# Optimization experiments

Measured on AMD Instinct MI355X. Metric: run time of the kernel, lower is better.

The kernel has to match this reference:

```python
import jax, jax.numpy as jnp
import numpy as np

Q_DIM = 256
CTX_DIM = 256
FF_DIM = 1024
B, LQ, LKV = 8, 2048, 4096


def setup_inputs() -> dict:
    key = jax.random.key(0)
    ks = jax.random.split(key, 16)
    s = lambda d: 1.0 / np.sqrt(d)
    return {
        "query": jax.random.normal(ks[0], (B, LQ, Q_DIM), jnp.float32),
        "key": jax.random.normal(ks[1], (B, LKV, CTX_DIM), jnp.float32),
        "value": jax.random.normal(ks[2], (B, LKV, CTX_DIM), jnp.float32),
        # attention projections (stored [in, out])
        "Wk": jax.random.normal(ks[3], (CTX_DIM, Q_DIM), jnp.float32) * s(CTX_DIM),
        "bk": jnp.zeros((Q_DIM,), jnp.float32),
        "Wv": jax.random.normal(ks[4], (CTX_DIM, Q_DIM), jnp.float32) * s(CTX_DIM),
        "bv": jnp.zeros((Q_DIM,), jnp.float32),
        "Wo": jax.random.normal(ks[5], (Q_DIM, Q_DIM), jnp.float32) * s(Q_DIM),
        "bo": jnp.zeros((Q_DIM,), jnp.float32),
        # layernorms
        "g1": jnp.ones((Q_DIM,), jnp.float32),
        "b1": jnp.zeros((Q_DIM,), jnp.float32),
        "g2": jnp.ones((Q_DIM,), jnp.float32),
        "b2": jnp.zeros((Q_DIM,), jnp.float32),
        # feedforward
        "W1": jax.random.normal(ks[6], (Q_DIM, FF_DIM), jnp.float32) * s(Q_DIM),
        "bf1": jnp.zeros((FF_DIM,), jnp.float32),
        "W2": jax.random.normal(ks[7], (FF_DIM, Q_DIM), jnp.float32) * s(FF_DIM),
        "bf2": jnp.zeros((Q_DIM,), jnp.float32),
    }


def _layernorm(x, g, b, eps=1e-5):
    mu = jnp.mean(x, axis=-1, keepdims=True)
    var = jnp.var(x, axis=-1, keepdims=True)
    return (x - mu) * jax.lax.rsqrt(var + eps) * g + b


def reference(query, key, value, Wk, bk, Wv, bv, Wo, bo, g1, b1, g2, b2, W1, bf1, W2, bf2):
    # CrossAttention (single-head, naive)
    key_proj = key @ Wk + bk        # [B, Lkv, D]
    value_proj = value @ Wv + bv    # [B, Lkv, D]
    scale = 1.0 / jnp.sqrt(jnp.asarray(Q_DIM, query.dtype))
    scores = jnp.einsum("bqd,bkd->bqk", query, key_proj) * scale  # [B, Lq, Lkv]
    weights = jax.nn.softmax(scores, axis=-1)
    context = jnp.einsum("bqk,bkd->bqd", weights, value_proj)     # [B, Lq, D]
    attn_out = context @ Wo + bo
    # residual + LN
    x = _layernorm(query + attn_out, g1, b1)
    # FeedForward (condition_dim=0, dropout=0)
    ff = jax.nn.relu(x @ W1 + bf1) @ W2 + bf2
    return _layernorm(x + ff, g2, b2)
```

## Files before the change

kernel.cpp:

```cpp
#include <hip/hip_runtime.h>
#include <stdint.h>

typedef __attribute__((ext_vector_type(4))) float f32x4;
typedef __attribute__((ext_vector_type(16))) float f32x16;
typedef __attribute__((ext_vector_type(8))) short short8;
typedef __attribute__((ext_vector_type(4))) short short4v;
typedef __attribute__((ext_vector_type(4))) unsigned uint4v;

__device__ __forceinline__ short f2bf(float f) {
  union { float f; uint32_t u; } v; v.f = f;
  uint32_t r = v.u + 0x7FFFu + ((v.u >> 16) & 1u);
  return (short)(r >> 16);
}

__device__ __forceinline__ float bf2f(short s) {
  union { unsigned u; float f; } v; v.u = ((unsigned)(unsigned short)s) << 16; return v.f;
}

__device__ __forceinline__ unsigned cvt_pk_bf16(float lo, float hi) {
  unsigned r;
  asm("v_cvt_pk_bf16_f32 %0, %1, %2" : "=v"(r) : "v"(lo), "v"(hi));
  return r;
}

__device__ __forceinline__ void pl32swap(unsigned& x, unsigned& y) {
  asm volatile("v_permlane32_swap_b32 %0, %1" : "+v"(x), "+v"(y));
}

__device__ __forceinline__ f32x4 mfma16(short8 a, short8 b, f32x4 c) {
  return __builtin_amdgcn_mfma_f32_16x16x32_bf16(a, b, c, 0, 0, 0);
}
__device__ __forceinline__ f32x16 mfma32(short8 a, short8 b, f32x16 c) {
  return __builtin_amdgcn_mfma_f32_32x32x16_bf16(a, b, c, 0, 0, 0);
}

#define NB 8
#define LQ 2048
#define LKV 4096
#define DQ 256
#define FF 1024
#define NCHUNK 2
#define ROWS (NB * LQ)

#define AS1(p) ((const __attribute__((address_space(1))) void*)(p))
#define AS3(p) ((__attribute__((address_space(3))) void*)(p))

__global__ void transpose_all(
    const float* __restrict__ Wk, const float* __restrict__ Wv,
    const float* __restrict__ Wo, const float* __restrict__ W1,
    const float* __restrict__ W2,
    short* __restrict__ WkT, short* __restrict__ WvT, short* __restrict__ WoT,
    short* __restrict__ W1T, short* __restrict__ W2T) {
  __shared__ float t[32][33];
  int bid = blockIdx.x;
  const float* in; short* out; int R, C, b0;
  if (bid < 64)       { in = Wk; out = WkT; R = 256;  C = 256;  b0 = bid; }
  else if (bid < 128) { in = Wv; out = WvT; R = 256;  C = 256;  b0 = bid - 64; }
  else if (bid < 192) { in = Wo; out = WoT; R = 256;  C = 256;  b0 = bid - 128; }
  else if (bid < 448) { in = W1; out = W1T; R = 256;  C = 1024; b0 = bid - 192; }
  else                { in = W2; out = W2T; R = 1024; C = 256;  b0 = bid - 448; }
  int nbx = C / 32;
  int c0 = (b0 % nbx) * 32, r0 = (b0 / nbx) * 32;
  int tx = threadIdx.x, ty = threadIdx.y;
#pragma unroll
  for (int dy = 0; dy < 32; dy += 8)
    t[ty + dy][tx] = in[(long)(r0 + ty + dy) * C + c0 + tx];
  __syncthreads();
#pragma unroll
  for (int dy = 0; dy < 32; dy += 8)
    out[(long)(c0 + ty + dy) * R + r0 + tx] = f2bf(t[tx][ty + dy]);
}

template <int AMODE, int BMODE, int EPI>
__global__ void __launch_bounds__(256, 2) gemm128(
    const void* __restrict__ A, long sAb, int lda,
    const void* __restrict__ B, long sBb, int ldb,
    const float* __restrict__ bias,
    void* C, long sCb, int ldc, int K) {
  __shared__ char lds[32768];
  const int tid = threadIdx.x;
  const int bn = blockIdx.x, bm = blockIdx.y, bz = blockIdx.z;
  const int w = tid >> 6, l = tid & 63;
  const int wm = w & 1, wn = w >> 1;
  const int lr = l & 15, lq = l >> 4;

  auto stageReg = [&](const float* src, int ld, long row0, int k0, char* ldsb) {
#pragma unroll
    for (int it = 0; it < 4; ++it) {
      int idx = it * 2048 + tid * 8;
      int r = idx >> 6, c = idx & 63;
      const float* p = src + (row0 + r) * (long)ld + k0 + c;
      f32x4 f0 = *(const f32x4*)p, f1 = *(const f32x4*)(p + 4);
      uint4v u;
      u[0] = cvt_pk_bf16(f0[0], f0[1]); u[1] = cvt_pk_bf16(f0[2], f0[3]);
      u[2] = cvt_pk_bf16(f1[0], f1[1]); u[3] = cvt_pk_bf16(f1[2], f1[3]);
      *(short8*)(ldsb + ((r * 128 + c * 2) ^ ((r & 7) << 4))) = *(short8*)&u;
    }
  };
  auto stageGld = [&](const short* src, int ld, long row0, int k0, char* ldsb) {
#pragma unroll
    for (int it = 0; it < 4; ++it) {
      const int span = it * 4096 + w * 1024;
      int idx = (span >> 4) + l;
      int r = idx >> 3, c = idx & 7;
      __builtin_amdgcn_global_load_lds(
          AS1(src + (row0 + r) * (long)ld + k0 + ((c ^ (r & 7)) * 8)),
          AS3(ldsb + span), 16, 0, 0);
    }
  };

  f32x4 acc[4][4] = {};
  for (int k0 = 0; k0 < K; k0 += 64) {
    if (AMODE == 0)      stageGld((const short*)A + sAb * bz, lda, (long)bm * 128, k0, lds);
    else                 stageReg((const float*)A + sAb * bz, lda, (long)bm * 128, k0, lds);
    if (BMODE == 0)      stageGld((const short*)B + sBb * bz, ldb, (long)bn * 128, k0, lds + 16384);
    else                 stageReg((const float*)B + sBb * bz, ldb, (long)bn * 128, k0, lds + 16384);
    __syncthreads();
    short8 af[4][2], bfr[4][2];
#pragma unroll
    for (int i = 0; i < 4; ++i) {
#pragma unroll
      for (int kk = 0; kk < 2; ++kk) {
        int ra = wm * 64 + i * 16 + lr;
        af[i][kk] = *(const short8*)(lds + ((ra * 128 + (kk * 32 + lq * 8) * 2) ^ ((ra & 7) << 4)));
        int rb = wn * 64 + i * 16 + lr;
        bfr[i][kk] = *(const short8*)(lds + 16384 + ((rb * 128 + (kk * 32 + lq * 8) * 2) ^ ((rb & 7) << 4)));
      }
    }
#pragma unroll
    for (int i = 0; i < 4; ++i)
#pragma unroll
      for (int j = 0; j < 4; ++j) {
        acc[i][j] = mfma16(af[i][0], bfr[j][0], acc[i][j]);
        acc[i][j] = mfma16(af[i][1], bfr[j][1], acc[i][j]);
      }
    __syncthreads();
  }
#pragma unroll
  for (int i = 0; i < 4; ++i) {
#pragma unroll
    for (int j = 0; j < 4; ++j) {
#pragma unroll
      for (int r = 0; r < 4; ++r) {
        long row = (long)bm * 128 + wm * 64 + i * 16 + lq * 4 + r;
        long col = (long)bn * 128 + wn * 64 + j * 16 + lr;
        float v = acc[i][j][r];
        if (EPI == 0) {
          v += bias[col];
          ((short*)C + sCb * bz)[row * ldc + col] = f2bf(v);
        } else if (EPI == 1) {
          v += bias[row];
          ((short*)C + sCb * bz)[row * ldc + col] = f2bf(v);
        } else {
          v += bias[col];
          v = fmaxf(v, 0.f);
          ((short*)C + sCb * bz)[row * ldc + col] = f2bf(v);
        }
      }
    }
  }
}

template <int AMODE, bool RESF32, bool WF32, bool WB16>
__global__ void __launch_bounds__(256, 2) gemmln(
    const void* __restrict__ A, const short* __restrict__ Bw,
    const float* __restrict__ bias, const void* __restrict__ resid,
    const float* __restrict__ Mcomb, const float* __restrict__ Lcomb,
    const float* __restrict__ g, const float* __restrict__ be,
    float* __restrict__ outF, short* __restrict__ outB, int K) {
  __shared__ char lds[40960];
  const int tid = threadIdx.x;
  const int bm = blockIdx.x;
  const int w = tid >> 6, l = tid & 63;
  const int lr = l & 15, lq = l >> 4;
  char* ldsA = lds;
  char* ldsB = lds + 8192;

  f32x4 acc[16] = {};
  for (int k0 = 0; k0 < K; k0 += 64) {
    if (AMODE == 0) {
      const short* src = (const short*)A;
#pragma unroll
      for (int it = 0; it < 2; ++it) {
        const int span = it * 4096 + w * 1024;
        int idx = (span >> 4) + l;
        int r = idx >> 3, c = idx & 7;
        __builtin_amdgcn_global_load_lds(
            AS1(src + ((long)bm * 64 + r) * K + k0 + ((c ^ (r & 7)) * 8)),
            AS3(ldsA + span), 16, 0, 0);
      }
    } else {
      const short* O0 = (const short*)A;
#pragma unroll
      for (int it = 0; it < 2; ++it) {
        int idx = it * 2048 + tid * 8;
        int r = idx >> 6, c = idx & 63;
        long row = (long)bm * 64 + r;
        float m0 = Mcomb[row], m1 = Mcomb[ROWS + row];
        float l0 = Lcomb[row], l1 = Lcomb[ROWS + row];
        float M = fmaxf(m0, m1);
        float e0 = exp2f(m0 - M) * l0, e1 = exp2f(m1 - M) * l1;
        float inv = 1.f / (e0 + e1);
        float w0 = e0 * inv, w1 = e1 * inv;
        const short* p0 = O0 + row * 256 + k0 + c;
        short8 v0 = *(const short8*)p0;
        short8 v1 = *(const short8*)(p0 + (long)ROWS * 256);
        uint4v u;
#pragma unroll
        for (int j = 0; j < 4; ++j) {
          float x0 = w0 * bf2f(v0[2 * j])     + w1 * bf2f(v1[2 * j]);
          float x1 = w0 * bf2f(v0[2 * j + 1]) + w1 * bf2f(v1[2 * j + 1]);
          u[j] = cvt_pk_bf16(x0, x1);
        }
        *(short8*)(ldsA + ((r * 128 + c * 2) ^ ((r & 7) << 4))) = *(short8*)&u;
      }
    }
#pragma unroll
    for (int it = 0; it < 8; ++it) {
      const int span = it * 4096 + w * 1024;
      int idx = (span >> 4) + l;
      int r = idx >> 3, c = idx & 7;
      __builtin_amdgcn_global_load_lds(
          AS1(Bw + (long)r * K + k0 + ((c ^ (r & 7)) * 8)),
          AS3(ldsB + span), 16, 0, 0);
    }
    __syncthreads();
    short8 af0, af1;
    {
      int ra = w * 16 + lr;
      af0 = *(const short8*)(ldsA + ((ra * 128 + (lq * 8) * 2) ^ ((ra & 7) << 4)));
      af1 = *(const short8*)(ldsA + ((ra * 128 + (32 + lq * 8) * 2) ^ ((ra & 7) << 4)));
    }
#pragma unroll
    for (int j = 0; j < 16; ++j) {
      int rb = j * 16 + lr;
      short8 b0 = *(const short8*)(ldsB + ((rb * 128 + (lq * 8) * 2) ^ ((rb & 7) << 4)));
      short8 b1 = *(const short8*)(ldsB + ((rb * 128 + (32 + lq * 8) * 2) ^ ((rb & 7) << 4)));
      acc[j] = mfma16(af0, b0, acc[j]);
      acc[j] = mfma16(af1, b1, acc[j]);
    }
    __syncthreads();
  }

  const long rowbase = (long)bm * 64 + w * 16;
  float bia[16], gg[16], bb[16];
#pragma unroll
  for (int j = 0; j < 16; ++j) {
    int col = j * 16 + lr;
    bia[j] = bias[col]; gg[j] = g[col]; bb[j] = be[col];
  }
#pragma unroll
  for (int r = 0; r < 4; ++r) {
    long row = rowbase + lq * 4 + r;
    float v[16];
    float s = 0.f, s2 = 0.f;
#pragma unroll
    for (int j = 0; j < 16; ++j) {
      long idx = row * 256 + j * 16 + lr;
      float rx = RESF32 ? ((const float*)resid)[idx] : bf2f(((const short*)resid)[idx]);
      float x = acc[j][r] + bia[j] + rx;
      v[j] = x; s += x; s2 += x * x;
    }
#pragma unroll
    for (int mk = 1; mk < 16; mk <<= 1) { s += __shfl_xor(s, mk); s2 += __shfl_xor(s2, mk); }
    float mu = s * (1.f / 256.f);
    float var = s2 * (1.f / 256.f) - mu * mu;
    float rstd = rsqrtf(var + 1e-5f);
#pragma unroll
    for (int j = 0; j < 16; ++j) {
      int col = j * 16 + lr;
      float y = (v[j] - mu) * rstd * gg[j] + bb[j];
      if (WF32) outF[row * 256 + col] = y;
      if (WB16) outB[row * 256 + col] = f2bf(y);
    }
  }
}

__global__ void __launch_bounds__(256, 1) flash_attn(
    const float* __restrict__ Q, const short* __restrict__ Kb,
    const short* __restrict__ Vt, short* __restrict__ Opart,
    float* __restrict__ Mb, float* __restrict__ Lb) {
  __shared__ char lds[131072];
  const int tid = threadIdx.x;
  const int n = blockIdx.x;
  const int b = n & 7;
  const int slot = n >> 3;
  const int qt = slot & 15;
  const int ch = slot >> 4;
  const int wid = tid >> 6, l = tid & 63;
  const int ql = l & 31, h = l >> 5;
  const int qrow0 = qt * 128 + wid * 32;
  const float* Qp = Q + ((long)b * LQ + qrow0 + ql) * DQ;
  const short* Kp = Kb + (long)b * LKV * DQ;
  const short* Vp = Vt + (long)b * DQ * LKV;
  const float SCQ = 0.0625f * 1.4426950408889634f;

  auto stage = [&](int bufb, int kv0) {
    char* kqb = lds + bufb * 65536;
    char* vtb = kqb + 32768;
#pragma unroll
    for (int i = 0; i < 8; ++i) {
      const int j = wid * 8192 + i * 1024;
      {
        int r = (j >> 9) + (l >> 5);
        int cc = l & 31;
        const short* gk = Kp + (long)(kv0 + r) * DQ + ((cc ^ (r & 15)) * 8);
        __builtin_amdgcn_global_load_lds(AS1(gk), AS3(kqb + j), 16, 0, 0);
      }
      {
        int d = (j >> 7) + (l >> 3);
        int cc = l & 7;
        const short* gv = Vp + (long)d * LKV + kv0 + ((cc ^ (d & 7)) * 8);
        __builtin_amdgcn_global_load_lds(AS1(gv), AS3(vtb + j), 16, 0, 0);
      }
    }
  };

  short8 qf[16];
#pragma unroll
  for (int w = 0; w < 16; ++w) {
    const float* p = Qp + w * 16 + h * 8;
    f32x4 f0 = *(const f32x4*)p, f1 = *(const f32x4*)(p + 4);
    short8 v;
#pragma unroll
    for (int j = 0; j < 4; ++j) { v[j] = f2bf(f0[j] * SCQ); v[4 + j] = f2bf(f1[j] * SCQ); }
    qf[w] = v;
  }

  f32x16 o[8] = {};
  float m_r = -1e30f, l_r = 0.f;

  const int kv_lo = ch * (LKV / NCHUNK);
  const int NT = (LKV / NCHUNK) / 64;

  stage(0, kv_lo);

  for (int t = 0; t < NT; ++t) {
    if (t + 1 < NT) {
      stage((t + 1) & 1, kv_lo + (t + 1) * 64);
      asm volatile("s_waitcnt vmcnt(16)" ::: "memory");
    } else {
      asm volatile("s_waitcnt vmcnt(0)" ::: "memory");
    }
    __builtin_amdgcn_s_barrier();
    __builtin_amdgcn_sched_barrier(0);
    char* kq = lds + (t & 1) * 65536;
    char* vt = kq + 32768;

    f32x16 sa = {}, sb = {};
    {
      const int krA = ql, krB = 32 + ql;
      const int baseA = krA * 512, swzA = (krA & 15) << 4;
      const int baseB = krB * 512, swzB = (krB & 15) << 4;
#pragma unroll
      for (int w = 0; w < 16; ++w) {
        short8 kfA = *(const short8*)(kq + ((baseA + w * 32 + h * 16) ^ swzA));
        sa = mfma32(kfA, qf[w], sa);
        short8 kfB = *(const short8*)(kq + ((baseB + w * 32 + h * 16) ^ swzB));
        sb = mfma32(kfB, qf[w], sb);
      }
    }

    {
      float m8[8];
#pragma unroll
      for (int i = 0; i < 8; ++i)
        m8[i] = fmaxf(fmaxf(sa[i], sa[i + 8]), fmaxf(sb[i], sb[i + 8]));
      float m0 = fmaxf(fmaxf(m8[0], m8[1]), fmaxf(m8[2], m8[3]));
      float m1 = fmaxf(fmaxf(m8[4], m8[5]), fmaxf(m8[6], m8[7]));
      float pmax = fmaxf(m0, m1);
      pmax = fmaxf(pmax, __shfl_xor(pmax, 32));
      if (__any(pmax > m_r + 8.f)) {
        float mn = fmaxf(m_r, pmax);
        float alpha = exp2f(m_r - mn);
        m_r = mn;
        l_r *= alpha;
#pragma unroll
        for (int rr = 0; rr < 16; ++rr) {
          int src = ((rr & 3) + 8 * (rr >> 2) + 4 * h) + 32 * h;
          float ar = __shfl(alpha, src);
#pragma unroll
          for (int nn = 0; nn < 8; ++nn) o[nn][rr] *= ar;
        }
      }
    }

    short8 paA[2], paB[2];
    float rs0 = 0.f, rs1 = 0.f, rs2 = 0.f, rs3 = 0.f;
    {
      float pA[16];
#pragma unroll
      for (int i = 0; i < 16; ++i) pA[i] = exp2f(sa[i] - m_r);
#pragma unroll
      for (int i = 0; i < 4; ++i) { rs0 += pA[4 * i]; rs1 += pA[4 * i + 1]; rs2 += pA[4 * i + 2]; rs3 += pA[4 * i + 3]; }
#pragma unroll
      for (int v = 0; v < 2; ++v) {
        unsigned w01 = cvt_pk_bf16(pA[8 * v + 0], pA[8 * v + 1]);
        unsigned w23 = cvt_pk_bf16(pA[8 * v + 2], pA[8 * v + 3]);
        unsigned w45 = cvt_pk_bf16(pA[8 * v + 4], pA[8 * v + 5]);
        unsigned w67 = cvt_pk_bf16(pA[8 * v + 6], pA[8 * v + 7]);
        pl32swap(w01, w45);
        pl32swap(w23, w67);
        uint4v u = {w01, w23, w45, w67};
        paA[v] = *(short8*)&u;
      }
    }
    {
      float pB[16];
#pragma unroll
      for (int i = 0; i < 16; ++i) pB[i] = exp2f(sb[i] - m_r);
#pragma unroll
      for (int i = 0; i < 4; ++i) { rs0 += pB[4 * i]; rs1 += pB[4 * i + 1]; rs2 += pB[4 * i + 2]; rs3 += pB[4 * i + 3]; }
#pragma unroll
      for (int v = 0; v < 2; ++v) {
        unsigned w01 = cvt_pk_bf16(pB[8 * v + 0], pB[8 * v + 1]);
        unsigned w23 = cvt_pk_bf16(pB[8 * v + 2], pB[8 * v + 3]);
        unsigned w45 = cvt_pk_bf16(pB[8 * v + 4], pB[8 * v + 5]);
        unsigned w67 = cvt_pk_bf16(pB[8 * v + 6], pB[8 * v + 7]);
        pl32swap(w01, w45);
        pl32swap(w23, w67);
        uint4v u = {w01, w23, w45, w67};
        paB[v] = *(short8*)&u;
      }
    }
    {
      float rs = (rs0 + rs1) + (rs2 + rs3);
      rs += __shfl_xor(rs, 32);
      l_r += rs;
    }

#pragma unroll
    for (int nn = 0; nn < 8; ++nn) {
      const int d = 32 * nn + ql;
      const int dbase = d * 128, dswz = (d & 7) << 4;
      short8 bv0 = *(const short8*)(vt + ((dbase + 0 * 32 + 16 * h) ^ dswz));
      o[nn] = mfma32(paA[0], bv0, o[nn]);
      short8 bv1 = *(const short8*)(vt + ((dbase + 1 * 32 + 16 * h) ^ dswz));
      o[nn] = mfma32(paA[1], bv1, o[nn]);
      short8 bv2 = *(const short8*)(vt + ((dbase + 2 * 32 + 16 * h) ^ dswz));
      o[nn] = mfma32(paB[0], bv2, o[nn]);
      short8 bv3 = *(const short8*)(vt + ((dbase + 3 * 32 + 16 * h) ^ dswz));
      o[nn] = mfma32(paB[1], bv3, o[nn]);
    }

    asm volatile("s_waitcnt lgkmcnt(0)" ::: "memory");
    __builtin_amdgcn_s_barrier();
    __builtin_amdgcn_sched_barrier(0);
  }

  const long rowb = (long)b * LQ + qrow0;
  float inv_l = 1.f / l_r;
#pragma unroll
  for (int rr = 0; rr < 16; ++rr) {
    int rloc = (rr & 3) + 8 * (rr >> 2) + 4 * h;
    float li = __shfl(inv_l, rloc + 32 * h);
    long grow = rowb + rloc;
    short* dst = Opart + ((long)ch * ROWS + grow) * 256 + ql;
#pragma unroll
    for (int nn = 0; nn < 8; ++nn) dst[32 * nn] = f2bf(o[nn][rr] * li);
  }
  if (h == 0) {
    Mb[(long)ch * ROWS + rowb + ql] = m_r;
    Lb[(long)ch * ROWS + rowb + ql] = l_r;
  }
}

extern "C" void kernel_launch(void* const* d_in, const int* in_sizes, int n_in,
                              void* d_out, int out_size, void* d_ws, size_t ws_size,
                              hipStream_t stream) {
  const float* query = (const float*)d_in[0];
  const float* key   = (const float*)d_in[1];
  const float* value = (const float*)d_in[2];
  const float* Wk  = (const float*)d_in[3];
  const float* bk  = (const float*)d_in[4];
  const float* Wv  = (const float*)d_in[5];
  const float* bv  = (const float*)d_in[6];
  const float* Wo  = (const float*)d_in[7];
  const float* bo  = (const float*)d_in[8];
  const float* g1  = (const float*)d_in[9];
  const float* b1  = (const float*)d_in[10];
  const float* g2  = (const float*)d_in[11];
  const float* b2  = (const float*)d_in[12];
  const float* W1  = (const float*)d_in[13];
  const float* bf1 = (const float*)d_in[14];
  const float* W2  = (const float*)d_in[15];
  const float* bf2 = (const float*)d_in[16];

  char* ws = (char*)d_ws;
  size_t off = 0;
  auto take = [&](size_t bytes) { char* p = ws + off; off += bytes; return p; };
  short* WkT = (short*)take((size_t)256 * 256 * 2);
  short* WvT = (short*)take((size_t)256 * 256 * 2);
  short* WoT = (short*)take((size_t)256 * 256 * 2);
  short* W1T = (short*)take((size_t)1024 * 256 * 2);
  short* W2T = (short*)take((size_t)256 * 1024 * 2);
  short* Kb  = (short*)take((size_t)NB * LKV * DQ * 2);
  short* Vt  = (short*)take((size_t)NB * DQ * LKV * 2);
  short* Opart = (short*)take((size_t)NCHUNK * ROWS * 256 * 2);
  float* Mbuf  = (float*)take((size_t)NCHUNK * ROWS * 4);
  float* Lbuf  = (float*)take((size_t)NCHUNK * ROWS * 4);
  short* Xb    = (short*)take((size_t)ROWS * 256 * 2);
  short* Hb  = (short*)Kb;
  (void)ws_size; (void)in_sizes; (void)n_in; (void)out_size;

  dim3 blk(256);
  transpose_all<<<dim3(704), dim3(32, 8), 0, stream>>>(
      Wk, Wv, Wo, W1, W2, WkT, WvT, WoT, W1T, W2T);

  gemm128<1, 0, 0><<<dim3(2, 256, 1), blk, 0, stream>>>(
      key, 0, 256, WkT, 0, 256, bk, Kb, 0, 256, 256);
  gemm128<0, 1, 1><<<dim3(32, 2, 8), blk, 0, stream>>>(
      WvT, 0, 256, value, (long)LKV * 256, 256, bv, Vt, (long)256 * LKV, LKV, 256);
  flash_attn<<<dim3(256), blk, 0, stream>>>(query, Kb, Vt, Opart, Mbuf, Lbuf);
  gemmln<2, true, false, true><<<dim3(ROWS / 64), blk, 0, stream>>>(
      Opart, WoT, bo, query, Mbuf, Lbuf, g1, b1, nullptr, Xb, 256);
  gemm128<0, 0, 3><<<dim3(8, 128, 1), blk, 0, stream>>>(
      Xb, 0, 256, W1T, 0, 256, bf1, Hb, 0, 1024, 256);
  gemmln<0, false, true, false><<<dim3(ROWS / 64), blk, 0, stream>>>(
      Hb, W2T, bf2, Xb, nullptr, nullptr, g2, b2, (float*)d_out, nullptr, 1024);
}
```

Measured before the change: 222.2 us.

## Double-buffer LDS staging in gemmln for the direct-load A mode

For AMODE 0, the gemmln kernel now splits LDS into two 40 KB buffers and prefetches the next K-slice of A and the weights with global_load_lds while the current slice runs through MFMA. It uses a partial vmcnt wait and raw s_barrier calls in place of two __syncthreads per iteration. The goal is to hide global-load latency behind compute. In exchange, LDS per block doubles to 80 KB, which may cut the two-blocks-per-CU occupancy set by the launch bounds.

```diff
diff --git a/kernel.cpp b/kernel.cpp
--- a/kernel.cpp
+++ b/kernel.cpp
@@ -168,53 +168,25 @@
     const float* __restrict__ Mcomb, const float* __restrict__ Lcomb,
     const float* __restrict__ g, const float* __restrict__ be,
     float* __restrict__ outF, short* __restrict__ outB, int K) {
-  __shared__ char lds[40960];
+  __shared__ char lds[(AMODE == 0) ? 81920 : 40960];
   const int tid = threadIdx.x;
   const int bm = blockIdx.x;
   const int w = tid >> 6, l = tid & 63;
   const int lr = l & 15, lq = l >> 4;
-  char* ldsA = lds;
-  char* ldsB = lds + 8192;
-
-  f32x4 acc[16] = {};
-  for (int k0 = 0; k0 < K; k0 += 64) {
-    if (AMODE == 0) {
-      const short* src = (const short*)A;
-#pragma unroll
-      for (int it = 0; it < 2; ++it) {
-        const int span = it * 4096 + w * 1024;
-        int idx = (span >> 4) + l;
-        int r = idx >> 3, c = idx & 7;
-        __builtin_amdgcn_global_load_lds(
-            AS1(src + ((long)bm * 64 + r) * K + k0 + ((c ^ (r & 7)) * 8)),
-            AS3(ldsA + span), 16, 0, 0);
-      }
-    } else {
-      const short* O0 = (const short*)A;
-#pragma unroll
-      for (int it = 0; it < 2; ++it) {
-        int idx = it * 2048 + tid * 8;
-        int r = idx >> 6, c = idx & 63;
-        long row = (long)bm * 64 + r;
-        float m0 = Mcomb[row], m1 = Mcomb[ROWS + row];
-        float l0 = Lcomb[row], l1 = Lcomb[ROWS + row];
-        float M = fmaxf(m0, m1);
-        float e0 = exp2f(m0 - M) * l0, e1 = exp2f(m1 - M) * l1;
-        float inv = 1.f / (e0 + e1);
-        float w0 = e0 * inv, w1 = e1 * inv;
-        const short* p0 = O0 + row * 256 + k0 + c;
-        short8 v0 = *(const short8*)p0;
-        short8 v1 = *(const short8*)(p0 + (long)ROWS * 256);
-        uint4v u;
-#pragma unroll
-        for (int j = 0; j < 4; ++j) {
-          float x0 = w0 * bf2f(v0[2 * j])     + w1 * bf2f(v1[2 * j]);
-          float x1 = w0 * bf2f(v0[2 * j + 1]) + w1 * bf2f(v1[2 * j + 1]);
-          u[j] = cvt_pk_bf16(x0, x1);
-        }
-        *(short8*)(ldsA + ((r * 128 + c * 2) ^ ((r & 7) << 4))) = *(short8*)&u;
-      }
-    }
+
+  auto stageA0 = [&](int k0, char* ldsA) {
+    const short* src = (const short*)A;
+#pragma unroll
+    for (int it = 0; it < 2; ++it) {
+      const int span = it * 4096 + w * 1024;
+      int idx = (span >> 4) + l;
+      int r = idx >> 3, c = idx & 7;
+      __builtin_amdgcn_global_load_lds(
+          AS1(src + ((long)bm * 64 + r) * K + k0 + ((c ^ (r & 7)) * 8)),
+          AS3(ldsA + span), 16, 0, 0);
+    }
+  };
+  auto stageB = [&](int k0, char* ldsB) {
 #pragma unroll
     for (int it = 0; it < 8; ++it) {
       const int span = it * 4096 + w * 1024;
@@ -224,13 +196,39 @@
           AS1(Bw + (long)r * K + k0 + ((c ^ (r & 7)) * 8)),
           AS3(ldsB + span), 16, 0, 0);
     }
-    __syncthreads();
+  };
+  auto stageA2 = [&](int k0, char* ldsA) {
+    const short* O0 = (const short*)A;
+#pragma unroll
+    for (int it = 0; it < 2; ++it) {
+      int idx = it * 2048 + tid * 8;
+      int r = idx >> 6, c = idx & 63;
+      long row = (long)bm * 64 + r;
+      float m0 = Mcomb[row], m1 = Mcomb[ROWS + row];
+      float l0 = Lcomb[row], l1 = Lcomb[ROWS + row];
+      float M = fmaxf(m0, m1);
+      float e0 = exp2f(m0 - M) * l0, e1 = exp2f(m1 - M) * l1;
+      float inv = 1.f / (e0 + e1);
+      float w0 = e0 * inv, w1 = e1 * inv;
+      const short* p0 = O0 + row * 256 + k0 + c;
+      short8 v0 = *(const short8*)p0;
+      short8 v1 = *(const short8*)(p0 + (long)ROWS * 256);
+      uint4v u;
+#pragma unroll
+      for (int j = 0; j < 4; ++j) {
+        float x0 = w0 * bf2f(v0[2 * j])     + w1 * bf2f(v1[2 * j]);
+        float x1 = w0 * bf2f(v0[2 * j + 1]) + w1 * bf2f(v1[2 * j + 1]);
+        u[j] = cvt_pk_bf16(x0, x1);
+      }
+      *(short8*)(ldsA + ((r * 128 + c * 2) ^ ((r & 7) << 4))) = *(short8*)&u;
+    }
+  };
+
+  auto compute = [&](char* ldsA, char* ldsB, f32x4* acc) {
     short8 af0, af1;
-    {
-      int ra = w * 16 + lr;
-      af0 = *(const short8*)(ldsA + ((ra * 128 + (lq * 8) * 2) ^ ((ra & 7) << 4)));
-      af1 = *(const short8*)(ldsA + ((ra * 128 + (32 + lq * 8) * 2) ^ ((ra & 7) << 4)));
-    }
+    int ra = w * 16 + lr;
+    af0 = *(const short8*)(ldsA + ((ra * 128 + (lq * 8) * 2) ^ ((ra & 7) << 4)));
+    af1 = *(const short8*)(ldsA + ((ra * 128 + (32 + lq * 8) * 2) ^ ((ra & 7) << 4)));
 #pragma unroll
     for (int j = 0; j < 16; ++j) {
       int rb = j * 16 + lr;
@@ -239,7 +237,38 @@
       acc[j] = mfma16(af0, b0, acc[j]);
       acc[j] = mfma16(af1, b1, acc[j]);
     }
-    __syncthreads();
+  };
+
+  f32x4 acc[16] = {};
+  if (AMODE == 0) {
+    const int NS = K / 64;
+    stageA0(0, lds);
+    stageB(0, lds + 8192);
+    for (int ks = 0; ks < NS; ++ks) {
+      if (ks + 1 < NS) {
+        char* nbuf = lds + ((ks + 1) & 1) * 40960;
+        stageA0((ks + 1) * 64, nbuf);
+        stageB((ks + 1) * 64, nbuf + 8192);
+        asm volatile("s_waitcnt vmcnt(10)" ::: "memory");
+      } else {
+        asm volatile("s_waitcnt vmcnt(0)" ::: "memory");
+      }
+      __builtin_amdgcn_s_barrier();
+      __builtin_amdgcn_sched_barrier(0);
+      char* buf = lds + (ks & 1) * 40960;
+      compute(buf, buf + 8192, acc);
+      asm volatile("s_waitcnt lgkmcnt(0)" ::: "memory");
+      __builtin_amdgcn_s_barrier();
+      __builtin_amdgcn_sched_barrier(0);
+    }
+  } else {
+    for (int k0 = 0; k0 < K; k0 += 64) {
+      stageA2(k0, lds);
+      stageB(k0, lds + 8192);
+      __syncthreads();
+      compute(lds, lds + 8192, acc);
+      __syncthreads();
+    }
   }
 
   const long rowbase = (long)bm * 64 + w * 16;
```

New measurement: 214.0 us. 1.04x faster.
